# Optimization experiments

Hardware: AMD Instinct MI355X
Metric: run time of the kernel (lower is better)

## Reference

```python
import jax, jax.numpy as jnp
import numpy as np
from jax import lax

F_, W_, H_ = -0.01, -0.1, 1.0
K5 = np.array([[F_]*5, [F_, W_, W_, W_, F_], [F_, W_, H_, W_, F_], [F_, W_, W_, W_, F_], [F_]*5], dtype=np.float32)
K3 = np.array([[W_, W_, W_], [W_, H_, W_], [W_, W_, W_]], dtype=np.float32)


def depthwise_conv(x, k2d):
    # x: [B,C,H,W]; same small kernel applied independently to every channel
    C = x.shape[1]
    kh = k2d.shape[0]
    kernel = jnp.broadcast_to(jnp.asarray(k2d, x.dtype)[None, None], (C, 1, kh, kh))
    pad = kh // 2
    return lax.conv_general_dilated(
        x, kernel,
        window_strides=(1, 1),
        padding=[(pad, pad), (pad, pad)],
        dimension_numbers=("NCHW", "OIHW", "NCHW"),
        feature_group_count=C,
    )


def maxpool5(x):
    # kernel_size=5, stride=1, padding=2 (torch MaxPool2d pads with -inf)
    return lax.reduce_window(
        x, -jnp.inf, lax.max,
        window_dimensions=(1, 1, 5, 5),
        window_strides=(1, 1, 1, 1),
        padding=[(0, 0), (0, 0), (2, 2), (2, 2)],
    )


def setup_inputs() -> dict:
    key = jax.random.key(0)
    x = jax.random.normal(key, (8, 64, 256, 256), dtype=jnp.float32)
    return {"x": x}


def reference(x):
    edge = depthwise_conv(x, K5) + depthwise_conv(x, K3)
    return jnp.abs(maxpool5(edge))
```

## Files before the change

### kernel.cpp

```cpp
#include <hip/hip_runtime.h>
#include <math.h>


#define TY 16
#define STEPS (TY + 8)

typedef float vfloat4 __attribute__((ext_vector_type(4)));

__global__ __launch_bounds__(256, 4)
void edgepool_kernel(const float* __restrict__ xin, float* __restrict__ yout) {
    const int lane  = threadIdx.x & 63;
    const int wave  = threadIdx.x >> 6;
    const int blk   = blockIdx.x;
    const int plane = blk >> 2;
    const int strip = ((blk & 3) << 2) | wave;
    const int y0    = strip * TY;

    const float4* __restrict__ in4  = (const float4*)xin + (size_t)plane * 16384;
    vfloat4*      __restrict__ out4 = (vfloat4*)    yout + (size_t)plane * 16384;

    const int nL = (lane == 0)  ? 0  : lane - 1;
    const int nR = (lane == 63) ? 63 : lane + 1;

    const float Wa = -0.01f, Wb = -0.19f, Wc = 2.2f;
    const float NINF = -INFINITY;

    float E[5][4];
    float V[5][4];
#pragma unroll
    for (int k = 0; k < 5; ++k)
#pragma unroll
        for (int j = 0; j < 4; ++j) { E[k][j] = 0.f; V[k][j] = NINF; }

#pragma unroll
    for (int t = 0; t < STEPS; ++t) {
        const int  r   = y0 - 4 + t;
        const bool rin = (unsigned)r < 256u;
        const int  rc  = rin ? r : (r < 0 ? 0 : 255);
        const float4 vC = in4[rc * 64 + lane];
        const float4 vL = in4[rc * 64 + nL];
        const float4 vR = in4[rc * 64 + nR];

        const float v0 = rin ? vC.x : 0.f;
        const float v1 = rin ? vC.y : 0.f;
        const float v2 = rin ? vC.z : 0.f;
        const float v3 = rin ? vC.w : 0.f;
        const float lm2 = (rin && lane != 0)  ? vL.z : 0.f;
        const float lm1 = (rin && lane != 0)  ? vL.w : 0.f;
        const float rp0 = (rin && lane != 63) ? vR.x : 0.f;
        const float rp1 = (rin && lane != 63) ? vR.y : 0.f;

        const float s01 = v0 + v1, s23 = v2 + v3;
        const float h3[4] = { lm1 + s01, s01 + v2, v1 + s23, s23 + rp0 };
        const float h5[4] = { lm2 + lm1 + s01 + v2, lm1 + s01 + s23,
                              s01 + s23 + rp0,      v1 + s23 + rp0 + rp1 };
        const float vv[4] = { v0, v1, v2, v3 };

        const int e2 = (t + 2) % 5, e1 = (t + 1) % 5, e0 = t % 5,
                  em1 = (t + 4) % 5, em2 = (t + 3) % 5;

#pragma unroll
        for (int j = 0; j < 4; ++j) {
            E[e2][j]  = Wa * h5[j];
            E[e1][j]  = fmaf(Wb, h3[j], fmaf(Wa, h5[j], E[e1][j]));
            E[e0][j]  = fmaf(Wc, vv[j], fmaf(Wb, h3[j], fmaf(Wa, h5[j], E[e0][j])));
            E[em1][j] = fmaf(Wb, h3[j], fmaf(Wa, h5[j], E[em1][j]));
            E[em2][j] = fmaf(Wa, h5[j], E[em2][j]);
        }

        const int  er  = r - 2;
        const bool ein = (unsigned)er < 256u;
        float e[4];
#pragma unroll
        for (int j = 0; j < 4; ++j) e[j] = ein ? E[em2][j] : NINF;

#pragma unroll
        for (int j = 0; j < 4; ++j) {
            V[e2][j]  = e[j];
            V[e1][j]  = fmaxf(V[e1][j], e[j]);
            V[e0][j]  = fmaxf(V[e0][j], e[j]);
            V[em1][j] = fmaxf(V[em1][j], e[j]);
            V[em2][j] = fmaxf(V[em2][j], e[j]);
        }

        if (t >= 8) {
            const float m0 = V[em2][0], m1 = V[em2][1], m2 = V[em2][2], m3 = V[em2][3];
            float ml2 = __shfl(m2, lane - 1, 64);
            float ml1 = __shfl(m3, lane - 1, 64);
            float mr0 = __shfl(m0, lane + 1, 64);
            float mr1 = __shfl(m1, lane + 1, 64);
            ml2 = (lane == 0)  ? NINF : ml2;
            ml1 = (lane == 0)  ? NINF : ml1;
            mr0 = (lane == 63) ? NINF : mr0;
            mr1 = (lane == 63) ? NINF : mr1;
            vfloat4 ov;
            ov.x = fabsf(fmaxf(fmaxf(ml2, ml1), fmaxf(fmaxf(m0, m1), m2)));
            ov.y = fabsf(fmaxf(fmaxf(ml1, m0), fmaxf(fmaxf(m1, m2), m3)));
            ov.z = fabsf(fmaxf(fmaxf(m0, m1), fmaxf(fmaxf(m2, m3), mr0)));
            ov.w = fabsf(fmaxf(fmaxf(m1, m2), fmaxf(fmaxf(m3, mr0), mr1)));
            __builtin_nontemporal_store(ov, &out4[(r - 4) * 64 + lane]);
        }
    }
}

extern "C" void kernel_launch(void* const* d_in, const int* in_sizes, int n_in,
                              void* d_out, int out_size, void* d_ws, size_t ws_size,
                              hipStream_t stream) {
    const float* x   = (const float*)d_in[0];
    float*       out = (float*)d_out;
    hipLaunchKernelGGL(edgepool_kernel, dim3(2048), dim3(256), 0, stream, x, out);
}
```

Measured before the change: 245.9 us.

## Prefetch all rows into registers, use shuffles for halo, halve strip height

```diff
diff --git a/kernel.cpp b/kernel.cpp
--- a/kernel.cpp
+++ b/kernel.cpp
@@ -2,7 +2,7 @@
 #include <math.h>
 
 
-#define TY 16
+#define TY 8
 #define STEPS (TY + 8)
 
 typedef float vfloat4 __attribute__((ext_vector_type(4)));
@@ -12,18 +12,23 @@
     const int lane  = threadIdx.x & 63;
     const int wave  = threadIdx.x >> 6;
     const int blk   = blockIdx.x;
-    const int plane = blk >> 2;
-    const int strip = ((blk & 3) << 2) | wave;
+    const int plane = blk >> 3;
+    const int strip = ((blk & 7) << 2) | wave;
     const int y0    = strip * TY;
 
     const float4* __restrict__ in4  = (const float4*)xin + (size_t)plane * 16384;
     vfloat4*      __restrict__ out4 = (vfloat4*)    yout + (size_t)plane * 16384;
 
-    const int nL = (lane == 0)  ? 0  : lane - 1;
-    const int nR = (lane == 63) ? 63 : lane + 1;
-
     const float Wa = -0.01f, Wb = -0.19f, Wc = 2.2f;
     const float NINF = -INFINITY;
+
+    float4 pf[STEPS];
+#pragma unroll
+    for (int t = 0; t < STEPS; ++t) {
+        const int r  = y0 - 4 + t;
+        const int rc = (r < 0) ? 0 : (r > 255 ? 255 : r);
+        pf[t] = in4[rc * 64 + lane];
+    }
 
     float E[5][4];
     float V[5][4];
@@ -36,19 +41,19 @@
     for (int t = 0; t < STEPS; ++t) {
         const int  r   = y0 - 4 + t;
         const bool rin = (unsigned)r < 256u;
-        const int  rc  = rin ? r : (r < 0 ? 0 : 255);
-        const float4 vC = in4[rc * 64 + lane];
-        const float4 vL = in4[rc * 64 + nL];
-        const float4 vR = in4[rc * 64 + nR];
+        const float v0 = rin ? pf[t].x : 0.f;
+        const float v1 = rin ? pf[t].y : 0.f;
+        const float v2 = rin ? pf[t].z : 0.f;
+        const float v3 = rin ? pf[t].w : 0.f;
 
-        const float v0 = rin ? vC.x : 0.f;
-        const float v1 = rin ? vC.y : 0.f;
-        const float v2 = rin ? vC.z : 0.f;
-        const float v3 = rin ? vC.w : 0.f;
-        const float lm2 = (rin && lane != 0)  ? vL.z : 0.f;
-        const float lm1 = (rin && lane != 0)  ? vL.w : 0.f;
-        const float rp0 = (rin && lane != 63) ? vR.x : 0.f;
-        const float rp1 = (rin && lane != 63) ? vR.y : 0.f;
+        float lm2 = __shfl(v2, lane - 1, 64);
+        float lm1 = __shfl(v3, lane - 1, 64);
+        float rp0 = __shfl(v0, lane + 1, 64);
+        float rp1 = __shfl(v1, lane + 1, 64);
+        lm2 = (lane == 0)  ? 0.f : lm2;
+        lm1 = (lane == 0)  ? 0.f : lm1;
+        rp0 = (lane == 63) ? 0.f : rp0;
+        rp1 = (lane == 63) ? 0.f : rp1;
 
         const float s01 = v0 + v1, s23 = v2 + v3;
         const float h3[4] = { lm1 + s01, s01 + v2, v1 + s23, s23 + rp0 };
@@ -108,5 +113,5 @@
                               hipStream_t stream) {
     const float* x   = (const float*)d_in[0];
     float*       out = (float*)d_out;
-    hipLaunchKernelGGL(edgepool_kernel, dim3(2048), dim3(256), 0, stream, x, out);
+    hipLaunchKernelGGL(edgepool_kernel, dim3(4096), dim3(256), 0, stream, x, out);
 }
```

Measured after the change: 231.4 us. 1.06x faster.
